# Kernel optimization log

Measured on AMD Instinct MI355X. Metric: run time of the kernel, lower is better.

Reference implementation:

```python
import jax, jax.numpy as jnp
import numpy as np

B, N_IN, NODE, L = 4, 128, 32, 256
N_HID, N_OUT = 64, 128
D_IN = N_HID          # d_inner = expand(1) * d_model
D_STATE = 2 * N_HID   # d_state = n_hid * 2
D_CONV = 2
DT_RANK = max(1, -(-N_HID // 16))  # ceil(d_model/16) = 4


def setup_inputs() -> dict:
    key = jax.random.key(0)
    ks = jax.random.split(key, 12)
    s = lambda k, shape, scale: (jax.random.normal(k, shape, jnp.float32) * scale)
    inputs = jax.random.normal(ks[0], (B, N_IN, NODE, L), jnp.float32)
    return {
        "inputs": inputs,
        "w_in": s(ks[1], (N_HID, N_IN), 1.0 / np.sqrt(N_IN)),
        "b_in": jnp.zeros((N_HID,), jnp.float32),
        "in_proj_w": s(ks[2], (2 * D_IN, N_HID), 1.0 / np.sqrt(N_HID)),
        "conv_w": s(ks[3], (D_IN, D_CONV), 0.5),
        "conv_b": jnp.zeros((D_IN,), jnp.float32),
        "x_proj_w": s(ks[4], (DT_RANK + 2 * D_STATE, D_IN), 1.0 / np.sqrt(D_IN)),
        "dt_proj_w": s(ks[5], (D_IN, DT_RANK), DT_RANK ** -0.5),
        "dt_proj_b": s(ks[6], (D_IN,), 0.1),
        "A_log": jnp.log(jnp.tile(jnp.arange(1, D_STATE + 1, dtype=jnp.float32)[None, :], (D_IN, 1))),
        "D": jnp.ones((D_IN,), jnp.float32),
        "out_proj_w": s(ks[7], (N_HID, D_IN), 1.0 / np.sqrt(D_IN)),
        "w_out": s(ks[8], (N_OUT, N_HID), 1.0 / np.sqrt(N_HID)),
        "b_out": jnp.zeros((N_OUT,), jnp.float32),
        "ln_w": jnp.ones((L, N_OUT), jnp.float32),
        "ln_b": jnp.zeros((L, N_OUT), jnp.float32),
    }


def _mamba(x, in_proj_w, conv_w, conv_b, x_proj_w, dt_proj_w, dt_proj_b, A_log, D, out_proj_w):
    # x: (Bseq, L, d_model)
    Bs, Ls, _ = x.shape
    d_state = A_log.shape[1]
    dt_rank = dt_proj_w.shape[1]
    d_conv = conv_w.shape[1]

    xz = x @ in_proj_w.T                     # (Bs, L, 2*d_inner)
    xm, z = jnp.split(xz, 2, axis=-1)

    # causal depthwise conv1d (padding = d_conv-1, truncated to L)
    xp = jnp.pad(xm, ((0, 0), (d_conv - 1, 0), (0, 0)))
    xc = sum(xp[:, k:k + Ls, :] * conv_w[:, k] for k in range(d_conv)) + conv_b
    xc = jax.nn.silu(xc)                     # (Bs, L, d_inner)

    dbc = xc @ x_proj_w.T                    # (Bs, L, dt_rank + 2*d_state)
    dt = dbc[..., :dt_rank]
    Bm = dbc[..., dt_rank:dt_rank + d_state]
    Cm = dbc[..., dt_rank + d_state:]
    delta = jax.nn.softplus(dt @ dt_proj_w.T + dt_proj_b)  # (Bs, L, d_inner)
    A = -jnp.exp(A_log)                      # (d_inner, d_state)

    def step(h, inp):
        dlt, Bt, Ct, xt = inp                # (Bs,d), (Bs,s), (Bs,s), (Bs,d)
        dA = jnp.exp(dlt[:, :, None] * A)    # (Bs, d, s)
        h = dA * h + (dlt * xt)[:, :, None] * Bt[:, None, :]
        y = jnp.einsum('bds,bs->bd', h, Ct)
        return h, y

    h0 = jnp.zeros((Bs, xm.shape[-1], d_state), x.dtype)
    xs = (delta.transpose(1, 0, 2), Bm.transpose(1, 0, 2),
          Cm.transpose(1, 0, 2), xc.transpose(1, 0, 2))
    _, ys = jax.lax.scan(step, h0, xs)       # ys: (L, Bs, d_inner)

    y = ys.transpose(1, 0, 2) + xc * D
    y = y * jax.nn.silu(z)
    return y @ out_proj_w.T                  # (Bs, L, d_model)


def reference(inputs, w_in, b_in, in_proj_w, conv_w, conv_b, x_proj_w,
              dt_proj_w, dt_proj_b, A_log, D, out_proj_w,
              w_out, b_out, ln_w, ln_b):
    b, n_in, node, seq = inputs.shape
    # permute(0,2,3,1).reshape(B*node, L, n_in)
    x = inputs.transpose(0, 2, 3, 1).reshape(b * node, seq, n_in)
    x = x @ w_in.T + b_in
    x = jax.nn.silu(_mamba(x, in_proj_w, conv_w, conv_b, x_proj_w,
                           dt_proj_w, dt_proj_b, A_log, D, out_proj_w))
    x = x @ w_out.T + b_out                  # (B*node, L, n_out)
    # LayerNorm over last two dims [feature_len, n_out]
    mu = x.mean(axis=(-2, -1), keepdims=True)
    var = ((x - mu) ** 2).mean(axis=(-2, -1), keepdims=True)
    x = (x - mu) / jnp.sqrt(var + 1e-5) * ln_w + ln_b
    return x.reshape(b, node, seq, -1).transpose(0, 3, 1, 2)
```

## Files before the change

kernel.cpp:

```cpp
#include <hip/hip_runtime.h>
#include <math.h>


__device__ __forceinline__ float silu_f(float v) { return v / (1.f + __expf(-v)); }
__device__ __forceinline__ float softplus_f(float v) { return v > 20.f ? v : log1pf(__expf(v)); }

__global__ __launch_bounds__(256) void k1_proj(
    const float* __restrict__ inp, const float* __restrict__ w_in,
    const float* __restrict__ b_in, const float* __restrict__ ipw,
    float* __restrict__ XM, float* __restrict__ Zb)
{
  __shared__ float sIN[128*64];
  __shared__ float sW[64*68];
  __shared__ float sXT[64*68];
  const int bid = blockIdx.x;
  const int r = bid >> 2, tb = bid & 3;
  const int b = r >> 5, node = r & 31;
  const int t0 = tb * 64;
  const int tid = threadIdx.x;
  const int tg = tid & 15, vg = tid >> 4;
  const int tl0 = tg * 4, v0 = vg * 4;

  for (int e = tid; e < 128*64; e += 256) {
    int i = e >> 6, t = e & 63;
    sIN[e] = inp[((b*128 + i)*32 + node)*256 + t0 + t];
  }

  float acc[4][4];
  #pragma unroll
  for (int ti = 0; ti < 4; ti++)
    #pragma unroll
    for (int j = 0; j < 4; j++) acc[ti][j] = b_in[v0 + j];

  for (int kc = 0; kc < 2; kc++) {
    __syncthreads();
    for (int e = tid; e < 64*16; e += 256) {
      int row = e >> 4, c4 = e & 15;
      *(float4*)&sW[row*68 + c4*4] = *(const float4*)&w_in[row*128 + kc*64 + c4*4];
    }
    __syncthreads();
    for (int k4 = 0; k4 < 16; k4++) {
      float4 wv[4];
      #pragma unroll
      for (int j = 0; j < 4; j++)
        wv[j] = *(const float4*)&sW[(v0 + j)*68 + k4*4];
      #pragma unroll
      for (int kk = 0; kk < 4; kk++) {
        float4 x4 = *(const float4*)&sIN[(kc*64 + k4*4 + kk)*64 + tl0];
        #pragma unroll
        for (int j = 0; j < 4; j++) {
          float w = kk==0 ? wv[j].x : kk==1 ? wv[j].y : kk==2 ? wv[j].z : wv[j].w;
          acc[0][j] = fmaf(x4.x, w, acc[0][j]);
          acc[1][j] = fmaf(x4.y, w, acc[1][j]);
          acc[2][j] = fmaf(x4.z, w, acc[2][j]);
          acc[3][j] = fmaf(x4.w, w, acc[3][j]);
        }
      }
    }
  }
  #pragma unroll
  for (int j = 0; j < 4; j++)
    *(float4*)&sXT[(v0 + j)*68 + tl0] =
        make_float4(acc[0][j], acc[1][j], acc[2][j], acc[3][j]);

  for (int pass = 0; pass < 2; pass++) {
    __syncthreads();
    for (int e = tid; e < 64*16; e += 256) {
      int row = e >> 4, c4 = e & 15;
      *(float4*)&sW[row*68 + c4*4] = *(const float4*)&ipw[(pass*64 + row)*64 + c4*4];
    }
    __syncthreads();

    float a2[4][4];
    #pragma unroll
    for (int ti = 0; ti < 4; ti++)
      #pragma unroll
      for (int j = 0; j < 4; j++) a2[ti][j] = 0.f;

    for (int k4 = 0; k4 < 16; k4++) {
      float4 wv[4];
      #pragma unroll
      for (int j = 0; j < 4; j++)
        wv[j] = *(const float4*)&sW[(v0 + j)*68 + k4*4];
      #pragma unroll
      for (int kk = 0; kk < 4; kk++) {
        float4 x4 = *(const float4*)&sXT[(k4*4 + kk)*68 + tl0];
        #pragma unroll
        for (int j = 0; j < 4; j++) {
          float w = kk==0 ? wv[j].x : kk==1 ? wv[j].y : kk==2 ? wv[j].z : wv[j].w;
          a2[0][j] = fmaf(x4.x, w, a2[0][j]);
          a2[1][j] = fmaf(x4.y, w, a2[1][j]);
          a2[2][j] = fmaf(x4.z, w, a2[2][j]);
          a2[3][j] = fmaf(x4.w, w, a2[3][j]);
        }
      }
    }

    float* dst = (pass == 0) ? XM : Zb;
    #pragma unroll
    for (int ti = 0; ti < 4; ti++)
      *(float4*)&dst[(r*256 + t0 + tl0 + ti)*64 + v0] =
          make_float4(a2[ti][0], a2[ti][1], a2[ti][2], a2[ti][3]);
  }
}

__global__ __launch_bounds__(256) void k2_conv_xproj(
    const float* __restrict__ XM, const float* __restrict__ convw,
    const float* __restrict__ convb, const float* __restrict__ xpw,
    const float* __restrict__ dtw, const float* __restrict__ dtb,
    float* __restrict__ XC, float* __restrict__ DELTA,
    float* __restrict__ BM, float* __restrict__ CM)
{
  __shared__ float sXM[65*64];
  __shared__ float sXC[64*68];
  __shared__ float sW[64*68];
  __shared__ float sDT[64*5];
  const int bid = blockIdx.x;
  const int r = bid >> 2, tb = bid & 3;
  const int t0 = tb * 64;
  const int tid = threadIdx.x;
  const int tg = tid & 15, vg = tid >> 4;
  const int tl0 = tg * 4, v0 = vg * 4;

  for (int e = tid; e < 65*64; e += 256) {
    int tt = e >> 6, d = e & 63;
    int tgl = t0 - 1 + tt;
    sXM[e] = (tgl < 0) ? 0.f : XM[(r*256 + tgl)*64 + d];
  }
  __syncthreads();

  for (int e = tid; e < 64*64; e += 256) {
    int t = e >> 6, d = e & 63;
    float c0 = convw[d*2], c1 = convw[d*2 + 1];
    float pre = fmaf(sXM[t*64 + d], c0, fmaf(sXM[(t+1)*64 + d], c1, convb[d]));
    float v = silu_f(pre);
    sXC[d*68 + t] = v;
    XC[(r*256 + t0 + t)*64 + d] = v;
  }

  for (int pass = 0; pass < 5; pass++) {
    __syncthreads();
    for (int e = tid; e < 64*16; e += 256) {
      int row = e >> 4, c4 = e & 15;
      int grow = pass*64 + row;
      float4 w = (grow < 260) ? *(const float4*)&xpw[grow*64 + c4*4]
                              : make_float4(0.f, 0.f, 0.f, 0.f);
      *(float4*)&sW[row*68 + c4*4] = w;
    }
    __syncthreads();

    float acc[4][4];
    #pragma unroll
    for (int ti = 0; ti < 4; ti++)
      #pragma unroll
      for (int jj = 0; jj < 4; jj++) acc[ti][jj] = 0.f;

    for (int k4 = 0; k4 < 16; k4++) {
      float4 wv[4];
      #pragma unroll
      for (int jj = 0; jj < 4; jj++)
        wv[jj] = *(const float4*)&sW[(v0 + jj)*68 + k4*4];
      #pragma unroll
      for (int kk = 0; kk < 4; kk++) {
        float4 x4 = *(const float4*)&sXC[(k4*4 + kk)*68 + tl0];
        #pragma unroll
        for (int jj = 0; jj < 4; jj++) {
          float w = kk==0 ? wv[jj].x : kk==1 ? wv[jj].y : kk==2 ? wv[jj].z : wv[jj].w;
          acc[0][jj] = fmaf(x4.x, w, acc[0][jj]);
          acc[1][jj] = fmaf(x4.y, w, acc[1][jj]);
          acc[2][jj] = fmaf(x4.z, w, acc[2][jj]);
          acc[3][jj] = fmaf(x4.w, w, acc[3][jj]);
        }
      }
    }

    const int j0g = pass*64 + v0;
    if (j0g < 4) {
      #pragma unroll
      for (int ti = 0; ti < 4; ti++)
        #pragma unroll
        for (int jj = 0; jj < 4; jj++)
          sDT[(tl0 + ti)*5 + jj] = acc[ti][jj];
    } else if (j0g < 132) {
      #pragma unroll
      for (int ti = 0; ti < 4; ti++)
        *(float4*)&BM[(r*256 + t0 + tl0 + ti)*128 + (j0g - 4)] =
            make_float4(acc[ti][0], acc[ti][1], acc[ti][2], acc[ti][3]);
    } else if (j0g < 260) {
      #pragma unroll
      for (int ti = 0; ti < 4; ti++)
        *(float4*)&CM[(r*256 + t0 + tl0 + ti)*128 + (j0g - 132)] =
            make_float4(acc[ti][0], acc[ti][1], acc[ti][2], acc[ti][3]);
    }
  }
  __syncthreads();

  for (int e = tid; e < 64*64; e += 256) {
    int t = e >> 6, d = e & 63;
    float4 w4 = *(const float4*)&dtw[d*4];
    float x = dtb[d];
    x = fmaf(sDT[t*5 + 0], w4.x, x);
    x = fmaf(sDT[t*5 + 1], w4.y, x);
    x = fmaf(sDT[t*5 + 2], w4.z, x);
    x = fmaf(sDT[t*5 + 3], w4.w, x);
    DELTA[(r*256 + t0 + t)*64 + d] = softplus_f(x);
  }
}

__global__ __launch_bounds__(256) void k3_scan(
    const float* __restrict__ DELTA, const float* __restrict__ XC,
    const float* __restrict__ BM, const float* __restrict__ CM,
    const float* __restrict__ alog, float* __restrict__ YP)
{
  __shared__ float sD[8*64], sX[8*64], sB[8*64], sC[8*64];
  const int bid = blockIdx.x;
  const int r = bid & 127, sc = bid >> 7;
  const int tid = threadIdx.x;
  const int dg = tid >> 4, sg = tid & 15;
  const int d0 = dg * 4, s0 = sc*64 + sg*4;

  float a[4][4], h[4][4];
  #pragma unroll
  for (int i = 0; i < 4; i++)
    #pragma unroll
    for (int j = 0; j < 4; j++) {
      a[i][j] = -expf(alog[(d0 + i)*128 + s0 + j]);
      h[i][j] = 0.f;
    }

  for (int tb = 0; tb < 32; tb++) {
    for (int e = tid; e < 512; e += 256) {
      int tt = e >> 6, q = e & 63;
      int t = tb*8 + tt;
      sD[e] = DELTA[(r*256 + t)*64 + q];
      sX[e] = XC[(r*256 + t)*64 + q];
      sB[e] = BM[(r*256 + t)*128 + sc*64 + q];
      sC[e] = CM[(r*256 + t)*128 + sc*64 + q];
    }
    __syncthreads();

    #pragma unroll
    for (int tt = 0; tt < 8; tt++) {
      float4 dl4 = *(const float4*)&sD[tt*64 + d0];
      float4 xc4 = *(const float4*)&sX[tt*64 + d0];
      float4 B4  = *(const float4*)&sB[tt*64 + sg*4];
      float4 C4  = *(const float4*)&sC[tt*64 + sg*4];
      float dl[4] = {dl4.x, dl4.y, dl4.z, dl4.w};
      float xc[4] = {xc4.x, xc4.y, xc4.z, xc4.w};
      float Bv[4] = {B4.x, B4.y, B4.z, B4.w};
      float Cv[4] = {C4.x, C4.y, C4.z, C4.w};
      float y[4];
      #pragma unroll
      for (int i = 0; i < 4; i++) {
        float u = dl[i] * xc[i];
        float yp = 0.f;
        #pragma unroll
        for (int j = 0; j < 4; j++) {
          float dA = __expf(dl[i] * a[i][j]);
          h[i][j] = fmaf(dA, h[i][j], u * Bv[j]);
          yp = fmaf(h[i][j], Cv[j], yp);
        }
        y[i] = yp;
      }
      #pragma unroll
      for (int i = 0; i < 4; i++) {
        float yp = y[i];
        yp += __shfl_xor(yp, 1);
        yp += __shfl_xor(yp, 2);
        yp += __shfl_xor(yp, 4);
        yp += __shfl_xor(yp, 8);
        y[i] = yp;
      }
      if (sg == 0) {
        int t = tb*8 + tt;
        float4 v = make_float4(y[0], y[1], y[2], y[3]);
        *(float4*)&YP[((sc*128 + r)*256 + t)*64 + d0] = v;
      }
    }
    __syncthreads();
  }
}

__global__ __launch_bounds__(256) void k4_post(
    const float* __restrict__ YP, const float* __restrict__ XC,
    const float* __restrict__ Zb, const float* __restrict__ Dp,
    const float* __restrict__ opw, const float* __restrict__ wout,
    const float* __restrict__ bout, float* __restrict__ out,
    float* __restrict__ PSTAT)
{
  __shared__ float sY[64*68];
  __shared__ float sU[64*68];
  __shared__ float sW[64*68];
  __shared__ float sRs[256], sRq[256];
  const int bid = blockIdx.x;
  const int r = bid >> 2, tb = bid & 3;
  const int b = r >> 5, node = r & 31;
  const int t0 = tb * 64;
  const int tid = threadIdx.x;
  const int tg = tid & 15, vg = tid >> 4;
  const int tl0 = tg * 4, v0 = vg * 4;

  for (int e = tid; e < 64*64; e += 256) {
    int t = e >> 6, d = e & 63;
    int idx = (r*256 + t0 + t)*64 + d;
    float y = YP[idx] + YP[2097152 + idx];
    float y2 = fmaf(XC[idx], Dp[d], y);
    sY[d*68 + t] = y2 * silu_f(Zb[idx]);
  }

  __syncthreads();
  for (int e = tid; e < 64*16; e += 256) {
    int row = e >> 4, c4 = e & 15;
    *(float4*)&sW[row*68 + c4*4] = *(const float4*)&opw[row*64 + c4*4];
  }
  __syncthreads();

  {
    float acc[4][4];
    #pragma unroll
    for (int ti = 0; ti < 4; ti++)
      #pragma unroll
      for (int j = 0; j < 4; j++) acc[ti][j] = 0.f;
    for (int k4 = 0; k4 < 16; k4++) {
      float4 wv[4];
      #pragma unroll
      for (int j = 0; j < 4; j++)
        wv[j] = *(const float4*)&sW[(v0 + j)*68 + k4*4];
      #pragma unroll
      for (int kk = 0; kk < 4; kk++) {
        float4 x4 = *(const float4*)&sY[(k4*4 + kk)*68 + tl0];
        #pragma unroll
        for (int j = 0; j < 4; j++) {
          float w = kk==0 ? wv[j].x : kk==1 ? wv[j].y : kk==2 ? wv[j].z : wv[j].w;
          acc[0][j] = fmaf(x4.x, w, acc[0][j]);
          acc[1][j] = fmaf(x4.y, w, acc[1][j]);
          acc[2][j] = fmaf(x4.z, w, acc[2][j]);
          acc[3][j] = fmaf(x4.w, w, acc[3][j]);
        }
      }
    }
    #pragma unroll
    for (int j = 0; j < 4; j++)
      *(float4*)&sU[(v0 + j)*68 + tl0] =
          make_float4(silu_f(acc[0][j]), silu_f(acc[1][j]),
                      silu_f(acc[2][j]), silu_f(acc[3][j]));
  }

  float s = 0.f, q = 0.f;
  for (int pass = 0; pass < 2; pass++) {
    __syncthreads();
    for (int e = tid; e < 64*16; e += 256) {
      int row = e >> 4, c4 = e & 15;
      *(float4*)&sW[row*68 + c4*4] = *(const float4*)&wout[(pass*64 + row)*64 + c4*4];
    }
    __syncthreads();

    float a2[4][4];
    #pragma unroll
    for (int ti = 0; ti < 4; ti++)
      #pragma unroll
      for (int j = 0; j < 4; j++) a2[ti][j] = bout[pass*64 + v0 + j];

    for (int k4 = 0; k4 < 16; k4++) {
      float4 wv[4];
      #pragma unroll
      for (int j = 0; j < 4; j++)
        wv[j] = *(const float4*)&sW[(v0 + j)*68 + k4*4];
      #pragma unroll
      for (int kk = 0; kk < 4; kk++) {
        float4 x4 = *(const float4*)&sU[(k4*4 + kk)*68 + tl0];
        #pragma unroll
        for (int j = 0; j < 4; j++) {
          float w = kk==0 ? wv[j].x : kk==1 ? wv[j].y : kk==2 ? wv[j].z : wv[j].w;
          a2[0][j] = fmaf(x4.x, w, a2[0][j]);
          a2[1][j] = fmaf(x4.y, w, a2[1][j]);
          a2[2][j] = fmaf(x4.z, w, a2[2][j]);
          a2[3][j] = fmaf(x4.w, w, a2[3][j]);
        }
      }
    }

    #pragma unroll
    for (int ti = 0; ti < 4; ti++)
      #pragma unroll
      for (int j = 0; j < 4; j++) {
        float v = a2[ti][j];
        s += v;
        q = fmaf(v, v, q);
      }
    #pragma unroll
    for (int j = 0; j < 4; j++) {
      int o = pass*64 + v0 + j;
      *(float4*)&out[((b*128 + o)*32 + node)*256 + t0 + tl0] =
          make_float4(a2[0][j], a2[1][j], a2[2][j], a2[3][j]);
    }
  }

  sRs[tid] = s; sRq[tid] = q;
  __syncthreads();
  for (int st = 128; st > 0; st >>= 1) {
    if (tid < st) { sRs[tid] += sRs[tid + st]; sRq[tid] += sRq[tid + st]; }
    __syncthreads();
  }
  if (tid == 0) { PSTAT[bid*2] = sRs[0]; PSTAT[bid*2 + 1] = sRq[0]; }
}

__global__ __launch_bounds__(256) void k5_ln(
    const float* __restrict__ PSTAT, const float* __restrict__ lnw,
    const float* __restrict__ lnb, float* __restrict__ out)
{
  __shared__ float sLW[32*129], sLB[32*129];
  const int bid = blockIdx.x;
  const int r = bid >> 3, tb = bid & 7;
  const int b = r >> 5, node = r & 31;
  const int t0 = tb * 32;
  const int tid = threadIdx.x;

  float s = 0.f, q = 0.f;
  #pragma unroll
  for (int p = 0; p < 4; p++) {
    s += PSTAT[(r*4 + p)*2];
    q += PSTAT[(r*4 + p)*2 + 1];
  }
  const float mu = s * (1.f / 32768.f);
  const float var = q * (1.f / 32768.f) - mu * mu;
  const float rstd = rsqrtf(var + 1e-5f);

  for (int e = tid; e < 32*128; e += 256) {
    int t = e >> 7, o = e & 127;
    sLW[t*129 + o] = lnw[(t0 + t)*128 + o];
    sLB[t*129 + o] = lnb[(t0 + t)*128 + o];
  }
  __syncthreads();

  for (int n = 0; n < 16; n++) {
    int t = tid & 31;
    int o = (tid >> 5) + n*8;
    int idx = ((b*128 + o)*32 + node)*256 + t0 + t;
    float v = out[idx];
    out[idx] = fmaf((v - mu) * rstd, sLW[t*129 + o], sLB[t*129 + o]);
  }
}

extern "C" void kernel_launch(void* const* d_in, const int* in_sizes, int n_in,
                              void* d_out, int out_size, void* d_ws, size_t ws_size,
                              hipStream_t stream)
{
  (void)in_sizes; (void)n_in; (void)out_size; (void)ws_size;
  const float* inp   = (const float*)d_in[0];
  const float* w_in  = (const float*)d_in[1];
  const float* b_in  = (const float*)d_in[2];
  const float* ipw   = (const float*)d_in[3];
  const float* convw = (const float*)d_in[4];
  const float* convb = (const float*)d_in[5];
  const float* xpw   = (const float*)d_in[6];
  const float* dtw   = (const float*)d_in[7];
  const float* dtb   = (const float*)d_in[8];
  const float* alog  = (const float*)d_in[9];
  const float* Dp    = (const float*)d_in[10];
  const float* opw   = (const float*)d_in[11];
  const float* wout  = (const float*)d_in[12];
  const float* bout  = (const float*)d_in[13];
  const float* lnw   = (const float*)d_in[14];
  const float* lnb   = (const float*)d_in[15];

  float* ws = (float*)d_ws;
  float* XM    = ws + 0;
  float* Zb    = ws + 2097152;
  float* XC    = ws + 4194304;
  float* DELTA = ws + 6291456;
  float* BM    = ws + 8388608;
  float* CM    = ws + 12582912;
  float* YP    = ws + 16777216;
  float* PSTAT = ws + 20971520;
  float* out   = (float*)d_out;

  k1_proj<<<dim3(512), dim3(256), 0, stream>>>(inp, w_in, b_in, ipw, XM, Zb);
  k2_conv_xproj<<<dim3(512), dim3(256), 0, stream>>>(XM, convw, convb, xpw, dtw, dtb,
                                                     XC, DELTA, BM, CM);
  k3_scan<<<dim3(256), dim3(256), 0, stream>>>(DELTA, XC, BM, CM, alog, YP);
  k4_post<<<dim3(512), dim3(256), 0, stream>>>(YP, XC, Zb, Dp, opw, wout, bout, out, PSTAT);
  k5_ln<<<dim3(1024), dim3(256), 0, stream>>>(PSTAT, lnw, lnb, out);
}
```

Baseline: 226.7 us.

## Split scan across d_inner chunks and prefetch next timestep tile into registers

The selective-scan kernel now splits the 64 inner channels into four chunks of 16 per block, which raises the grid from 256 to 1024 blocks. Each thread now holds one channel by four states instead of four by four. The next 8-timestep tile of B, C, delta and x is loaded into registers while the current tile is computed, then written to shared memory after a barrier. The aim is more parallelism across CUs for the serial scan and hiding of global load latency. The cost is that B and C tiles are reloaded by four times as many blocks, and each step does less work per thread while keeping the same shuffle reduction.

```diff
diff --git a/kernel.cpp b/kernel.cpp
--- a/kernel.cpp
+++ b/kernel.cpp
@@ -212,73 +212,97 @@
     const float* __restrict__ BM, const float* __restrict__ CM,
     const float* __restrict__ alog, float* __restrict__ YP)
 {
-  __shared__ float sD[8*64], sX[8*64], sB[8*64], sC[8*64];
+  __shared__ float sT[1280];
   const int bid = blockIdx.x;
-  const int r = bid & 127, sc = bid >> 7;
+  const int r = bid & 127;
+  const int rest = bid >> 7;
+  const int sc = rest & 1;
+  const int dc = rest >> 1;
   const int tid = threadIdx.x;
-  const int dg = tid >> 4, sg = tid & 15;
-  const int d0 = dg * 4, s0 = sc*64 + sg*4;
-
-  float a[4][4], h[4][4];
+  const int dg = tid >> 4;
+  const int sg = tid & 15;
+  const int sl0 = sg * 4;
+  const int d = dc*16 + dg;
+  const int sbase = sc*64 + sl0;
+
+  float a[4], h[4];
   #pragma unroll
-  for (int i = 0; i < 4; i++)
-    #pragma unroll
-    for (int j = 0; j < 4; j++) {
-      a[i][j] = -expf(alog[(d0 + i)*128 + s0 + j]);
-      h[i][j] = 0.f;
-    }
+  for (int j = 0; j < 4; j++) {
+    a[j] = -expf(alog[d*128 + sbase + j]);
+    h[j] = 0.f;
+  }
+
+  const float* baseB = BM + r*256*128 + sc*64;
+  const float* baseC = CM + r*256*128 + sc*64;
+  const float* baseD = DELTA + r*256*64 + dc*16;
+  const float* baseX = XC + r*256*64 + dc*16;
+
+  float pre0, pre1, pre2, pre3, pre4;
+  const int ttB = tid >> 6, qB = tid & 63;
+  const int ttD = (tid & 127) >> 4, qD = tid & 15;
+
+  #define K3_LOAD(tb_) do { \
+    int t0_ = (tb_)*8; \
+    pre0 = baseB[(t0_ + ttB)*128 + qB]; \
+    pre1 = baseB[(t0_ + 4 + ttB)*128 + qB]; \
+    pre2 = baseC[(t0_ + ttB)*128 + qB]; \
+    pre3 = baseC[(t0_ + 4 + ttB)*128 + qB]; \
+    pre4 = (tid < 128) ? baseD[(t0_ + ttD)*64 + qD] : baseX[(t0_ + ttD)*64 + qD]; \
+  } while (0)
+
+  #define K3_STORE() do { \
+    sT[ttB*64 + qB] = pre0; \
+    sT[(4 + ttB)*64 + qB] = pre1; \
+    sT[512 + ttB*64 + qB] = pre2; \
+    sT[512 + (4 + ttB)*64 + qB] = pre3; \
+    sT[((tid < 128) ? 1024 : 1152) + ttD*16 + qD] = pre4; \
+  } while (0)
+
+  K3_LOAD(0);
+  K3_STORE();
+  __syncthreads();
 
   for (int tb = 0; tb < 32; tb++) {
-    for (int e = tid; e < 512; e += 256) {
-      int tt = e >> 6, q = e & 63;
-      int t = tb*8 + tt;
-      sD[e] = DELTA[(r*256 + t)*64 + q];
-      sX[e] = XC[(r*256 + t)*64 + q];
-      sB[e] = BM[(r*256 + t)*128 + sc*64 + q];
-      sC[e] = CM[(r*256 + t)*128 + sc*64 + q];
-    }
-    __syncthreads();
+    if (tb < 31) K3_LOAD(tb + 1);
 
     #pragma unroll
     for (int tt = 0; tt < 8; tt++) {
-      float4 dl4 = *(const float4*)&sD[tt*64 + d0];
-      float4 xc4 = *(const float4*)&sX[tt*64 + d0];
-      float4 B4  = *(const float4*)&sB[tt*64 + sg*4];
-      float4 C4  = *(const float4*)&sC[tt*64 + sg*4];
-      float dl[4] = {dl4.x, dl4.y, dl4.z, dl4.w};
-      float xc[4] = {xc4.x, xc4.y, xc4.z, xc4.w};
-      float Bv[4] = {B4.x, B4.y, B4.z, B4.w};
-      float Cv[4] = {C4.x, C4.y, C4.z, C4.w};
-      float y[4];
-      #pragma unroll
-      for (int i = 0; i < 4; i++) {
-        float u = dl[i] * xc[i];
-        float yp = 0.f;
-        #pragma unroll
-        for (int j = 0; j < 4; j++) {
-          float dA = __expf(dl[i] * a[i][j]);
-          h[i][j] = fmaf(dA, h[i][j], u * Bv[j]);
-          yp = fmaf(h[i][j], Cv[j], yp);
-        }
-        y[i] = yp;
-      }
-      #pragma unroll
-      for (int i = 0; i < 4; i++) {
-        float yp = y[i];
-        yp += __shfl_xor(yp, 1);
-        yp += __shfl_xor(yp, 2);
-        yp += __shfl_xor(yp, 4);
-        yp += __shfl_xor(yp, 8);
-        y[i] = yp;
-      }
-      if (sg == 0) {
-        int t = tb*8 + tt;
-        float4 v = make_float4(y[0], y[1], y[2], y[3]);
-        *(float4*)&YP[((sc*128 + r)*256 + t)*64 + d0] = v;
-      }
-    }
-    __syncthreads();
-  }
+      float dl = sT[1024 + tt*16 + dg];
+      float xv = sT[1152 + tt*16 + dg];
+      float u  = dl * xv;
+      float4 Bv = *(const float4*)&sT[tt*64 + sl0];
+      float4 Cv = *(const float4*)&sT[512 + tt*64 + sl0];
+      float y = 0.f;
+      {
+        float dA0 = __expf(dl * a[0]);
+        h[0] = fmaf(dA0, h[0], u * Bv.x);
+        y = fmaf(h[0], Cv.x, y);
+        float dA1 = __expf(dl * a[1]);
+        h[1] = fmaf(dA1, h[1], u * Bv.y);
+        y = fmaf(h[1], Cv.y, y);
+        float dA2 = __expf(dl * a[2]);
+        h[2] = fmaf(dA2, h[2], u * Bv.z);
+        y = fmaf(h[2], Cv.z, y);
+        float dA3 = __expf(dl * a[3]);
+        h[3] = fmaf(dA3, h[3], u * Bv.w);
+        y = fmaf(h[3], Cv.w, y);
+      }
+      y += __shfl_xor(y, 1);
+      y += __shfl_xor(y, 2);
+      y += __shfl_xor(y, 4);
+      y += __shfl_xor(y, 8);
+      if (sg == 0)
+        YP[((sc*128 + r)*256 + tb*8 + tt)*64 + d] = y;
+    }
+
+    __syncthreads();
+    if (tb < 31) {
+      K3_STORE();
+      __syncthreads();
+    }
+  }
+  #undef K3_LOAD
+  #undef K3_STORE
 }
 
 __global__ __launch_bounds__(256) void k4_post(
@@ -478,7 +502,7 @@
   k1_proj<<<dim3(512), dim3(256), 0, stream>>>(inp, w_in, b_in, ipw, XM, Zb);
   k2_conv_xproj<<<dim3(512), dim3(256), 0, stream>>>(XM, convw, convb, xpw, dtw, dtb,
                                                      XC, DELTA, BM, CM);
-  k3_scan<<<dim3(256), dim3(256), 0, stream>>>(DELTA, XC, BM, CM, alog, YP);
+  k3_scan<<<dim3(1024), dim3(256), 0, stream>>>(DELTA, XC, BM, CM, alog, YP);
   k4_post<<<dim3(512), dim3(256), 0, stream>>>(YP, XC, Zb, Dp, opw, wout, bout, out, PSTAT);
   k5_ln<<<dim3(1024), dim3(256), 0, stream>>>(PSTAT, lnw, lnb, out);
 }
```

After: 185.7 us. 1.22x faster.
